# Kernel optimization log

Measured on AMD Instinct MI355X. Metric: run time of the kernel, lower is better.

Reference implementation:

```python
import jax, jax.numpy as jnp
import numpy as np

B, S, IN, OUT = 4, 2048, 4096, 11008


def setup_inputs() -> dict:
    key = jax.random.key(0)
    k1, k2, k3, k4, k5 = jax.random.split(key, 5)
    x = jax.random.normal(k1, (B, S, IN), dtype=jnp.float32)
    # int8 quantized weights, stored as int32 per harness spec but values in int8 range
    W_int8 = jax.random.randint(k2, (OUT, IN), -128, 128, dtype=jnp.int32)
    # per-output-channel scales (small positive) and zero-points
    scale = jax.random.uniform(k3, (OUT,), dtype=jnp.float32, minval=1e-3, maxval=2e-2)
    zero = jax.random.uniform(k4, (OUT,), dtype=jnp.float32, minval=-8.0, maxval=8.0)
    bias = jax.random.normal(k5, (OUT,), dtype=jnp.float32) * 0.01
    return {"x": x, "W_int8": W_int8, "scale": scale, "zero": zero, "bias": bias}


def reference(x, W_int8, scale, zero, bias):
    # Original torch forward raises on NaN/Inf in x; for valid inputs the math is
    # quant_matmul: dequantize W = (W_int8 - zero) * scale (per output channel),
    # then y = x @ W.T + bias.
    W = (W_int8.astype(jnp.float32) - zero[:, None]) * scale[:, None]  # [OUT, IN]
    y = jnp.einsum('bsi,oi->bso', x, W) + bias  # [B, S, OUT]
    return y
```

## Files before the change

### kernel.cpp

```cpp
#include <hip/hip_runtime.h>
#include <stdint.h>


#define M_DIM 8192
#define N_DIM 11008
#define K_DIM 4096
#define NT    (K_DIM / 128)
#define BUFB  65536

typedef __attribute__((ext_vector_type(4))) int i32x4;


__global__ void convert_w_kernel(const int* __restrict__ w,
                                 int8_t* __restrict__ o, int n4) {
  int idx = blockIdx.x * blockDim.x + threadIdx.x;
  int stride = gridDim.x * blockDim.x;
  for (int i = idx; i < n4; i += stride) {
    int4 v = ((const int4*)w)[i];
    int r = (v.x & 255) | ((v.y & 255) << 8) | ((v.z & 255) << 16) | ((v.w & 255) << 24);
    ((int*)o)[i] = r;
  }
}

__global__ __launch_bounds__(256) void quantx_kernel(
    const float* __restrict__ x, int8_t* __restrict__ h8, int8_t* __restrict__ l8,
    float* __restrict__ xs, float* __restrict__ rsum) {
  const int row = blockIdx.x;
  const int t = threadIdx.x;
  const float4* px = (const float4*)(x + (size_t)row * K_DIM);
  float4 v[4];
  float mx = 0.f, sm = 0.f;
  #pragma unroll
  for (int i = 0; i < 4; ++i) {
    v[i] = px[i * 256 + t];
    mx = fmaxf(mx, fmaxf(fmaxf(fabsf(v[i].x), fabsf(v[i].y)),
                         fmaxf(fabsf(v[i].z), fabsf(v[i].w))));
    sm += v[i].x + v[i].y + v[i].z + v[i].w;
  }
  #pragma unroll
  for (int off = 32; off > 0; off >>= 1) {
    mx = fmaxf(mx, __shfl_down(mx, off));
    sm += __shfl_down(sm, off);
  }
  __shared__ float rmx[4], rsm[4];
  const int wv = t >> 6, ln = t & 63;
  if (ln == 0) { rmx[wv] = mx; rsm[wv] = sm; }
  __syncthreads();
  const float rowmax = fmaxf(fmaxf(rmx[0], rmx[1]), fmaxf(rmx[2], rmx[3]));
  if (t == 0) {
    xs[row] = rowmax > 0.f ? rowmax / 16256.f : 0.f;
    rsum[row] = rsm[0] + rsm[1] + rsm[2] + rsm[3];
  }
  const float inv = rowmax > 0.f ? 16256.f / rowmax : 0.f;
  int* hp = (int*)(h8 + (size_t)row * K_DIM);
  int* lp = (int*)(l8 + (size_t)row * K_DIM);
  #pragma unroll
  for (int i = 0; i < 4; ++i) {
    int q0 = (int)rintf(v[i].x * inv);
    int q1 = (int)rintf(v[i].y * inv);
    int q2 = (int)rintf(v[i].z * inv);
    int q3 = (int)rintf(v[i].w * inv);
    int h0 = (q0 + 64) >> 7, h1 = (q1 + 64) >> 7, h2 = (q2 + 64) >> 7, h3 = (q3 + 64) >> 7;
    int l0 = q0 - (h0 << 7), l1 = q1 - (h1 << 7), l2 = q2 - (h2 << 7), l3 = q3 - (h3 << 7);
    hp[i * 256 + t] = (h0 & 255) | ((h1 & 255) << 8) | ((h2 & 255) << 16) | ((h3 & 255) << 24);
    lp[i * 256 + t] = (l0 & 255) | ((l1 & 255) << 8) | ((l2 & 255) << 16) | ((l3 & 255) << 24);
  }
}


__device__ __forceinline__ void stage_tile(
    const int8_t* __restrict__ Ah, const int8_t* __restrict__ Al,
    const int8_t* __restrict__ Bw, size_t a_base, size_t b_base,
    int ks, int srow, int scol, int wave, int8_t* buf) {
  #pragma unroll
  for (int r = 0; r < 2; ++r) {
    const int8_t* g = Ah + a_base + (size_t)(r * 64 + srow) * K_DIM + ks + scol;
    __builtin_amdgcn_global_load_lds((const __attribute__((address_space(1))) void*)g,
        (__attribute__((address_space(3))) void*)(buf + r * 8192 + wave * 1024), 16, 0, 0);
  }
  #pragma unroll
  for (int r = 0; r < 2; ++r) {
    const int8_t* g = Al + a_base + (size_t)(r * 64 + srow) * K_DIM + ks + scol;
    __builtin_amdgcn_global_load_lds((const __attribute__((address_space(1))) void*)g,
        (__attribute__((address_space(3))) void*)(buf + 16384 + r * 8192 + wave * 1024), 16, 0, 0);
  }
  #pragma unroll
  for (int r = 0; r < 4; ++r) {
    const int8_t* g = Bw + b_base + (size_t)(r * 64 + srow) * K_DIM + ks + scol;
    __builtin_amdgcn_global_load_lds((const __attribute__((address_space(1))) void*)g,
        (__attribute__((address_space(3))) void*)(buf + 32768 + r * 8192 + wave * 1024), 16, 0, 0);
  }
}

__global__ __launch_bounds__(512, 2) void qgemm_kernel(
    const int8_t* __restrict__ Ah, const int8_t* __restrict__ Al,
    const int8_t* __restrict__ Bw, const float* __restrict__ xs,
    const float* __restrict__ rowsum, const float* __restrict__ scale,
    const float* __restrict__ zero, const float* __restrict__ bias,
    float* __restrict__ out) {
  extern __shared__ int8_t smem[];

  const int tid = threadIdx.x;
  const int wave = tid >> 6;
  const int lane = tid & 63;

  const int bid = blockIdx.x;
  const int wg = (bid & 7) * 344 + (bid >> 3);
  const int group = wg / 344;
  const int rem = wg % 344;
  const int bm = group * 8 + (rem & 7);
  const int bn = rem >> 3;

  const int wr = wave >> 2;
  const int wc = wave & 3;

  i32x4 acch[4][4], accl[4][4];
  #pragma unroll
  for (int i = 0; i < 4; ++i)
    #pragma unroll
    for (int j = 0; j < 4; ++j) {
      acch[i][j] = (i32x4){0, 0, 0, 0};
      accl[i][j] = (i32x4){0, 0, 0, 0};
    }

  const int srow = tid >> 3;
  const int scol = (((tid & 7) ^ ((tid >> 3) & 7)) << 4);
  const size_t a_base = (size_t)(bm * 128) * K_DIM;
  const size_t b_base = (size_t)((size_t)bn * 256) * K_DIM;

  const int fr = lane & 15;
  const int g = lane >> 4;
  const int sw = fr & 7;
  const int sc0 = ((g ^ sw) << 4);
  const int sc1 = (((g + 4) ^ sw) << 4);

  stage_tile(Ah, Al, Bw, a_base, b_base, 0, srow, scol, wave, smem);
  asm volatile("s_waitcnt vmcnt(0)" ::: "memory");
  asm volatile("s_barrier" ::: "memory");

  for (int t = 0; t < NT; ++t) {
    if (t + 1 < NT) {
      stage_tile(Ah, Al, Bw, a_base, b_base, (t + 1) * 128, srow, scol, wave,
                 smem + ((t + 1) & 1) * BUFB);
      asm volatile("s_waitcnt vmcnt(8)" ::: "memory");
    } else {
      asm volatile("s_waitcnt vmcnt(0)" ::: "memory");
    }
    asm volatile("s_barrier" ::: "memory");

    const int8_t* buf = smem + (t & 1) * BUFB;
    const int8_t* ldsAh_ = buf;
    const int8_t* ldsAl_ = buf + 16384;
    const int8_t* ldsB_  = buf + 32768;

    #pragma unroll
    for (int h = 0; h < 2; ++h) {
      const int sc = h ? sc1 : sc0;
      i32x4 bfrag[4];
      #pragma unroll
      for (int ni = 0; ni < 4; ++ni) {
        const int row = wc * 64 + ni * 16 + fr;
        bfrag[ni] = *(const i32x4*)(ldsB_ + row * 128 + sc);
      }
      #pragma unroll
      for (int mi = 0; mi < 4; ++mi) {
        const int arow = (wr * 64 + mi * 16 + fr) * 128 + sc;
        i32x4 ahf = *(const i32x4*)(ldsAh_ + arow);
        i32x4 alf = *(const i32x4*)(ldsAl_ + arow);
        #pragma unroll
        for (int ni = 0; ni < 4; ++ni) {
          acch[mi][ni] = __builtin_amdgcn_mfma_i32_16x16x64_i8(ahf, bfrag[ni], acch[mi][ni], 0, 0, 0);
          accl[mi][ni] = __builtin_amdgcn_mfma_i32_16x16x64_i8(alf, bfrag[ni], accl[mi][ni], 0, 0, 0);
        }
      }
    }
    asm volatile("s_barrier" ::: "memory");
  }

  const int row0 = bm * 128 + wr * 64;
  const int col0 = bn * 256 + wc * 64;
  float s_[4], sz_[4], b_[4];
  #pragma unroll
  for (int ni = 0; ni < 4; ++ni) {
    const int n = col0 + ni * 16 + fr;
    const float s = scale[n];
    s_[ni] = s;
    sz_[ni] = s * zero[n];
    b_[ni] = bias[n];
  }
  #pragma unroll
  for (int mi = 0; mi < 4; ++mi) {
    #pragma unroll
    for (int j = 0; j < 4; ++j) {
      const int m = row0 + mi * 16 + g * 4 + j;
      const float xsm = xs[m];
      const float rs = rowsum[m];
      float* po = out + (size_t)m * N_DIM + col0;
      #pragma unroll
      for (int ni = 0; ni < 4; ++ni) {
        const float G = xsm * (128.f * (float)acch[mi][ni][j] + (float)accl[mi][ni][j]);
        po[ni * 16 + fr] = s_[ni] * G - sz_[ni] * rs + b_[ni];
      }
    }
  }
}


__global__ void fallback_kernel(const float* __restrict__ x, const int* __restrict__ w,
                                const float* __restrict__ scale, const float* __restrict__ zero,
                                const float* __restrict__ bias, float* __restrict__ out) {
  const int n = blockIdx.x * 16 + (threadIdx.x & 15);
  const int m = blockIdx.y * 16 + (threadIdx.x >> 4);
  const float z = zero[n];
  const float* xr = x + (size_t)m * K_DIM;
  const int* wr = w + (size_t)n * K_DIM;
  float acc = 0.f;
  for (int k = 0; k < K_DIM; ++k) acc += xr[k] * ((float)wr[k] - z);
  out[(size_t)m * N_DIM + n] = scale[n] * acc + bias[n];
}


extern "C" void kernel_launch(void* const* d_in, const int* in_sizes, int n_in,
                              void* d_out, int out_size, void* d_ws, size_t ws_size,
                              hipStream_t stream) {
  const float* x     = (const float*)d_in[0];
  const int*   w     = (const int*)d_in[1];
  const float* scale = (const float*)d_in[2];
  const float* zero  = (const float*)d_in[3];
  const float* bias  = (const float*)d_in[4];
  float* out = (float*)d_out;

  const size_t n_x = (size_t)M_DIM * K_DIM;
  const size_t n_w = (size_t)N_DIM * K_DIM;
  const size_t need = n_x * 2 + n_w + (size_t)M_DIM * 8;

  if (ws_size < need) {
    dim3 gr(N_DIM / 16, M_DIM / 16);
    fallback_kernel<<<gr, 256, 0, stream>>>(x, w, scale, zero, bias, out);
    return;
  }

  int8_t* x_h = (int8_t*)d_ws;
  int8_t* x_l = x_h + n_x;
  int8_t* w_8 = x_l + n_x;
  float* rsum = (float*)(w_8 + n_w);
  float* xs   = rsum + M_DIM;

  convert_w_kernel<<<2048, 256, 0, stream>>>(w, w_8, (int)(n_w / 4));
  quantx_kernel<<<M_DIM, 256, 0, stream>>>(x, x_h, x_l, xs, rsum);

  (void)hipFuncSetAttribute((const void*)qgemm_kernel,
                            hipFuncAttributeMaxDynamicSharedMemorySize, 2 * BUFB);

  const int nblocks = (M_DIM / 128) * (N_DIM / 256);
  qgemm_kernel<<<nblocks, 512, 2 * BUFB, stream>>>(x_h, x_l, w_8, xs, rsum,
                                                   scale, zero, bias, out);
}
```

Baseline: 738.0 us.

## Split main loop into four barrier-separated phases with interleaved prefetch and setprio

Restructures the GEMM main loop into four sub-phases, each of which loads A/B fragments from LDS and then issues a batch of MFMAs. The prefetch of the next tile is split into an A part and a B part, issued in the first and second phases so that global loads overlap with compute. MFMA blocks are wrapped in s_setprio to favour math waves, and the vmcnt wait moves to the end of the iteration. This adds more barriers per iteration, which costs synchronisation overhead and relies on the compiler keeping the scheduling as written.

After: 736.5 us. About the same (-0.2%).

```diff
diff --git a/kernel.cpp b/kernel.cpp
--- a/kernel.cpp
+++ b/kernel.cpp
@@ -68,10 +68,9 @@
 }
 
 
-__device__ __forceinline__ void stage_tile(
+__device__ __forceinline__ void stage_A(
     const int8_t* __restrict__ Ah, const int8_t* __restrict__ Al,
-    const int8_t* __restrict__ Bw, size_t a_base, size_t b_base,
-    int ks, int srow, int scol, int wave, int8_t* buf) {
+    size_t a_base, int ks, int srow, int scol, int wave, int8_t* buf) {
   #pragma unroll
   for (int r = 0; r < 2; ++r) {
     const int8_t* g = Ah + a_base + (size_t)(r * 64 + srow) * K_DIM + ks + scol;
@@ -84,6 +83,11 @@
     __builtin_amdgcn_global_load_lds((const __attribute__((address_space(1))) void*)g,
         (__attribute__((address_space(3))) void*)(buf + 16384 + r * 8192 + wave * 1024), 16, 0, 0);
   }
+}
+
+__device__ __forceinline__ void stage_B(
+    const int8_t* __restrict__ Bw, size_t b_base,
+    int ks, int srow, int scol, int wave, int8_t* buf) {
   #pragma unroll
   for (int r = 0; r < 4; ++r) {
     const int8_t* g = Bw + b_base + (size_t)(r * 64 + srow) * K_DIM + ks + scol;
@@ -91,6 +95,9 @@
         (__attribute__((address_space(3))) void*)(buf + 32768 + r * 8192 + wave * 1024), 16, 0, 0);
   }
 }
+
+#define WAIT_LGKM0() do { asm volatile("s_waitcnt lgkmcnt(0)" ::: "memory"); \
+                          __builtin_amdgcn_sched_barrier(0); } while (0)
 
 __global__ __launch_bounds__(512, 2) void qgemm_kernel(
     const int8_t* __restrict__ Ah, const int8_t* __restrict__ Al,
@@ -134,47 +141,106 @@
   const int sc0 = ((g ^ sw) << 4);
   const int sc1 = (((g + 4) ^ sw) << 4);
 
-  stage_tile(Ah, Al, Bw, a_base, b_base, 0, srow, scol, wave, smem);
+  stage_A(Ah, Al, a_base, 0, srow, scol, wave, smem);
+  stage_B(Bw, b_base, 0, srow, scol, wave, smem);
   asm volatile("s_waitcnt vmcnt(0)" ::: "memory");
-  asm volatile("s_barrier" ::: "memory");
+  __builtin_amdgcn_s_barrier();
 
   for (int t = 0; t < NT; ++t) {
-    if (t + 1 < NT) {
-      stage_tile(Ah, Al, Bw, a_base, b_base, (t + 1) * 128, srow, scol, wave,
-                 smem + ((t + 1) & 1) * BUFB);
-      asm volatile("s_waitcnt vmcnt(8)" ::: "memory");
-    } else {
-      asm volatile("s_waitcnt vmcnt(0)" ::: "memory");
-    }
-    asm volatile("s_barrier" ::: "memory");
-
     const int8_t* buf = smem + (t & 1) * BUFB;
+    int8_t* nxt = smem + ((t + 1) & 1) * BUFB;
     const int8_t* ldsAh_ = buf;
     const int8_t* ldsAl_ = buf + 16384;
     const int8_t* ldsB_  = buf + 32768;
-
-    #pragma unroll
-    for (int h = 0; h < 2; ++h) {
-      const int sc = h ? sc1 : sc0;
-      i32x4 bfrag[4];
-      #pragma unroll
-      for (int ni = 0; ni < 4; ++ni) {
-        const int row = wc * 64 + ni * 16 + fr;
-        bfrag[ni] = *(const i32x4*)(ldsB_ + row * 128 + sc);
-      }
-      #pragma unroll
-      for (int mi = 0; mi < 4; ++mi) {
-        const int arow = (wr * 64 + mi * 16 + fr) * 128 + sc;
-        i32x4 ahf = *(const i32x4*)(ldsAh_ + arow);
-        i32x4 alf = *(const i32x4*)(ldsAl_ + arow);
-        #pragma unroll
-        for (int ni = 0; ni < 4; ++ni) {
-          acch[mi][ni] = __builtin_amdgcn_mfma_i32_16x16x64_i8(ahf, bfrag[ni], acch[mi][ni], 0, 0, 0);
-          accl[mi][ni] = __builtin_amdgcn_mfma_i32_16x16x64_i8(alf, bfrag[ni], accl[mi][ni], 0, 0, 0);
-        }
-      }
-    }
-    asm volatile("s_barrier" ::: "memory");
+    const bool pf = (t + 1 < NT);
+    const int nks = (t + 1) * 128;
+
+    i32x4 bfrag[4], af[2][2];
+
+    #pragma unroll
+    for (int ni = 0; ni < 4; ++ni)
+      bfrag[ni] = *(const i32x4*)(ldsB_ + (wc * 64 + ni * 16 + fr) * 128 + sc0);
+    #pragma unroll
+    for (int mi = 0; mi < 2; ++mi) {
+      const int arow = (wr * 64 + mi * 16 + fr) * 128 + sc0;
+      af[mi][0] = *(const i32x4*)(ldsAh_ + arow);
+      af[mi][1] = *(const i32x4*)(ldsAl_ + arow);
+    }
+    if (pf) stage_A(Ah, Al, a_base, nks, srow, scol, wave, nxt);
+    __builtin_amdgcn_s_barrier();
+    WAIT_LGKM0();
+    __builtin_amdgcn_s_setprio(1);
+    #pragma unroll
+    for (int mi = 0; mi < 2; ++mi)
+      #pragma unroll
+      for (int ni = 0; ni < 4; ++ni) {
+        acch[mi][ni] = __builtin_amdgcn_mfma_i32_16x16x64_i8(af[mi][0], bfrag[ni], acch[mi][ni], 0, 0, 0);
+        accl[mi][ni] = __builtin_amdgcn_mfma_i32_16x16x64_i8(af[mi][1], bfrag[ni], accl[mi][ni], 0, 0, 0);
+      }
+    __builtin_amdgcn_s_setprio(0);
+    __builtin_amdgcn_s_barrier();
+
+    #pragma unroll
+    for (int mi = 0; mi < 2; ++mi) {
+      const int arow = (wr * 64 + (mi + 2) * 16 + fr) * 128 + sc0;
+      af[mi][0] = *(const i32x4*)(ldsAh_ + arow);
+      af[mi][1] = *(const i32x4*)(ldsAl_ + arow);
+    }
+    if (pf) stage_B(Bw, b_base, nks, srow, scol, wave, nxt);
+    __builtin_amdgcn_s_barrier();
+    WAIT_LGKM0();
+    __builtin_amdgcn_s_setprio(1);
+    #pragma unroll
+    for (int mi = 0; mi < 2; ++mi)
+      #pragma unroll
+      for (int ni = 0; ni < 4; ++ni) {
+        acch[mi + 2][ni] = __builtin_amdgcn_mfma_i32_16x16x64_i8(af[mi][0], bfrag[ni], acch[mi + 2][ni], 0, 0, 0);
+        accl[mi + 2][ni] = __builtin_amdgcn_mfma_i32_16x16x64_i8(af[mi][1], bfrag[ni], accl[mi + 2][ni], 0, 0, 0);
+      }
+    __builtin_amdgcn_s_setprio(0);
+    __builtin_amdgcn_s_barrier();
+
+    #pragma unroll
+    for (int ni = 0; ni < 4; ++ni)
+      bfrag[ni] = *(const i32x4*)(ldsB_ + (wc * 64 + ni * 16 + fr) * 128 + sc1);
+    #pragma unroll
+    for (int mi = 0; mi < 2; ++mi) {
+      const int arow = (wr * 64 + mi * 16 + fr) * 128 + sc1;
+      af[mi][0] = *(const i32x4*)(ldsAh_ + arow);
+      af[mi][1] = *(const i32x4*)(ldsAl_ + arow);
+    }
+    __builtin_amdgcn_s_barrier();
+    WAIT_LGKM0();
+    __builtin_amdgcn_s_setprio(1);
+    #pragma unroll
+    for (int mi = 0; mi < 2; ++mi)
+      #pragma unroll
+      for (int ni = 0; ni < 4; ++ni) {
+        acch[mi][ni] = __builtin_amdgcn_mfma_i32_16x16x64_i8(af[mi][0], bfrag[ni], acch[mi][ni], 0, 0, 0);
+        accl[mi][ni] = __builtin_amdgcn_mfma_i32_16x16x64_i8(af[mi][1], bfrag[ni], accl[mi][ni], 0, 0, 0);
+      }
+    __builtin_amdgcn_s_setprio(0);
+    __builtin_amdgcn_s_barrier();
+
+    #pragma unroll
+    for (int mi = 0; mi < 2; ++mi) {
+      const int arow = (wr * 64 + (mi + 2) * 16 + fr) * 128 + sc1;
+      af[mi][0] = *(const i32x4*)(ldsAh_ + arow);
+      af[mi][1] = *(const i32x4*)(ldsAl_ + arow);
+    }
+    __builtin_amdgcn_s_barrier();
+    WAIT_LGKM0();
+    __builtin_amdgcn_s_setprio(1);
+    #pragma unroll
+    for (int mi = 0; mi < 2; ++mi)
+      #pragma unroll
+      for (int ni = 0; ni < 4; ++ni) {
+        acch[mi + 2][ni] = __builtin_amdgcn_mfma_i32_16x16x64_i8(af[mi][0], bfrag[ni], acch[mi + 2][ni], 0, 0, 0);
+        accl[mi + 2][ni] = __builtin_amdgcn_mfma_i32_16x16x64_i8(af[mi][1], bfrag[ni], accl[mi + 2][ni], 0, 0, 0);
+      }
+    __builtin_amdgcn_s_setprio(0);
+    asm volatile("s_waitcnt vmcnt(0)" ::: "memory");
+    __builtin_amdgcn_s_barrier();
   }
 
   const int row0 = bm * 128 + wr * 64;
```

## Switch to 32x32x32 int8 MFMA with software-pipelined LDS reads and interleaved prefetch

Applied to the files above, without the earlier changes.

Replaces the 16x16x64 int8 MFMA tiles with 32x32x32 MFMAs, giving each wave 2x2 tiles of 16-element accumulators. The K loop is restructured so that LDS fragment reads for the next sub-step are double-buffered in registers and overlap the MFMAs, with the global-to-LDS prefetch split into A and B halves interleaved between reads. Barriers drop from two per tile to one, and s_setprio is raised around the MFMA bursts. The epilogue indexing is rewritten for the 32x32 output layout. The risks are higher register pressure from the extra fragment buffers and a stall from the full vmcnt(0) wait each iteration.

Measured after the change: 786.2 us. 1.07x slower.

```diff
diff --git a/kernel.cpp b/kernel.cpp
--- a/kernel.cpp
+++ b/kernel.cpp
@@ -9,6 +9,7 @@
 #define BUFB  65536
 
 typedef __attribute__((ext_vector_type(4))) int i32x4;
+typedef __attribute__((ext_vector_type(16))) int i32x16;
 
 
 __global__ void convert_w_kernel(const int* __restrict__ w,
@@ -68,10 +69,9 @@
 }
 
 
-__device__ __forceinline__ void stage_tile(
+__device__ __forceinline__ void stage_A(
     const int8_t* __restrict__ Ah, const int8_t* __restrict__ Al,
-    const int8_t* __restrict__ Bw, size_t a_base, size_t b_base,
-    int ks, int srow, int scol, int wave, int8_t* buf) {
+    size_t a_base, int ks, int srow, int scol, int wave, int8_t* buf) {
   #pragma unroll
   for (int r = 0; r < 2; ++r) {
     const int8_t* g = Ah + a_base + (size_t)(r * 64 + srow) * K_DIM + ks + scol;
@@ -84,6 +84,11 @@
     __builtin_amdgcn_global_load_lds((const __attribute__((address_space(1))) void*)g,
         (__attribute__((address_space(3))) void*)(buf + 16384 + r * 8192 + wave * 1024), 16, 0, 0);
   }
+}
+
+__device__ __forceinline__ void stage_B(
+    const int8_t* __restrict__ Bw, size_t b_base,
+    int ks, int srow, int scol, int wave, int8_t* buf) {
   #pragma unroll
   for (int r = 0; r < 4; ++r) {
     const int8_t* g = Bw + b_base + (size_t)(r * 64 + srow) * K_DIM + ks + scol;
@@ -114,13 +119,13 @@
   const int wr = wave >> 2;
   const int wc = wave & 3;
 
-  i32x4 acch[4][4], accl[4][4];
-  #pragma unroll
-  for (int i = 0; i < 4; ++i)
+  i32x16 acch[2][2], accl[2][2];
+  #pragma unroll
+  for (int i = 0; i < 2; ++i)
     #pragma unroll
-    for (int j = 0; j < 4; ++j) {
-      acch[i][j] = (i32x4){0, 0, 0, 0};
-      accl[i][j] = (i32x4){0, 0, 0, 0};
+    for (int j = 0; j < 2; ++j) {
+      acch[i][j] = (i32x16)(0);
+      accl[i][j] = (i32x16)(0);
     }
 
   const int srow = tid >> 3;
@@ -128,78 +133,97 @@
   const size_t a_base = (size_t)(bm * 128) * K_DIM;
   const size_t b_base = (size_t)((size_t)bn * 256) * K_DIM;
 
-  const int fr = lane & 15;
-  const int g = lane >> 4;
-  const int sw = fr & 7;
-  const int sc0 = ((g ^ sw) << 4);
-  const int sc1 = (((g + 4) ^ sw) << 4);
-
-  stage_tile(Ah, Al, Bw, a_base, b_base, 0, srow, scol, wave, smem);
+  const int r31 = lane & 31;
+  const int g5 = lane >> 5;
+  const int sw = lane & 7;
+  int scb[4];
+  #pragma unroll
+  for (int s = 0; s < 4; ++s) scb[s] = (((2 * s + g5) ^ sw) << 4);
+
+  const int arow0 = (wr * 64 + r31) * 128;
+  const int arow1 = arow0 + 32 * 128;
+  const int brow0 = (wc * 64 + r31) * 128;
+  const int brow1 = brow0 + 32 * 128;
+
+#define RD_STEP(s, fa, fb) do {                                         \
+    fb[0]    = *(const i32x4*)(ldsB_  + brow0 + scb[s]);                \
+    fb[1]    = *(const i32x4*)(ldsB_  + brow1 + scb[s]);                \
+    fa[0][0] = *(const i32x4*)(ldsAh_ + arow0 + scb[s]);                \
+    fa[0][1] = *(const i32x4*)(ldsAl_ + arow0 + scb[s]);                \
+    fa[1][0] = *(const i32x4*)(ldsAh_ + arow1 + scb[s]);                \
+    fa[1][1] = *(const i32x4*)(ldsAl_ + arow1 + scb[s]);                \
+  } while (0)
+
+#define MM_STEP(fa, fb) do {                                                        \
+    __builtin_amdgcn_s_setprio(1);                                                  \
+    acch[0][0] = __builtin_amdgcn_mfma_i32_32x32x32_i8(fa[0][0], fb[0], acch[0][0], 0, 0, 0); \
+    accl[0][0] = __builtin_amdgcn_mfma_i32_32x32x32_i8(fa[0][1], fb[0], accl[0][0], 0, 0, 0); \
+    acch[0][1] = __builtin_amdgcn_mfma_i32_32x32x32_i8(fa[0][0], fb[1], acch[0][1], 0, 0, 0); \
+    accl[0][1] = __builtin_amdgcn_mfma_i32_32x32x32_i8(fa[0][1], fb[1], accl[0][1], 0, 0, 0); \
+    acch[1][0] = __builtin_amdgcn_mfma_i32_32x32x32_i8(fa[1][0], fb[0], acch[1][0], 0, 0, 0); \
+    accl[1][0] = __builtin_amdgcn_mfma_i32_32x32x32_i8(fa[1][1], fb[0], accl[1][0], 0, 0, 0); \
+    acch[1][1] = __builtin_amdgcn_mfma_i32_32x32x32_i8(fa[1][0], fb[1], acch[1][1], 0, 0, 0); \
+    accl[1][1] = __builtin_amdgcn_mfma_i32_32x32x32_i8(fa[1][1], fb[1], accl[1][1], 0, 0, 0); \
+    __builtin_amdgcn_s_setprio(0);                                                  \
+  } while (0)
+
+  stage_A(Ah, Al, a_base, 0, srow, scol, wave, smem);
+  stage_B(Bw, b_base, 0, srow, scol, wave, smem);
   asm volatile("s_waitcnt vmcnt(0)" ::: "memory");
-  asm volatile("s_barrier" ::: "memory");
+  __builtin_amdgcn_s_barrier();
+
+  i32x4 fa0[2][2], fb0[2], fa1[2][2], fb1[2];
 
   for (int t = 0; t < NT; ++t) {
-    if (t + 1 < NT) {
-      stage_tile(Ah, Al, Bw, a_base, b_base, (t + 1) * 128, srow, scol, wave,
-                 smem + ((t + 1) & 1) * BUFB);
-      asm volatile("s_waitcnt vmcnt(8)" ::: "memory");
-    } else {
-      asm volatile("s_waitcnt vmcnt(0)" ::: "memory");
-    }
-    asm volatile("s_barrier" ::: "memory");
-
     const int8_t* buf = smem + (t & 1) * BUFB;
+    int8_t* nxt = smem + ((t + 1) & 1) * BUFB;
     const int8_t* ldsAh_ = buf;
     const int8_t* ldsAl_ = buf + 16384;
     const int8_t* ldsB_  = buf + 32768;
-
-    #pragma unroll
-    for (int h = 0; h < 2; ++h) {
-      const int sc = h ? sc1 : sc0;
-      i32x4 bfrag[4];
-      #pragma unroll
-      for (int ni = 0; ni < 4; ++ni) {
-        const int row = wc * 64 + ni * 16 + fr;
-        bfrag[ni] = *(const i32x4*)(ldsB_ + row * 128 + sc);
-      }
-      #pragma unroll
-      for (int mi = 0; mi < 4; ++mi) {
-        const int arow = (wr * 64 + mi * 16 + fr) * 128 + sc;
-        i32x4 ahf = *(const i32x4*)(ldsAh_ + arow);
-        i32x4 alf = *(const i32x4*)(ldsAl_ + arow);
-        #pragma unroll
-        for (int ni = 0; ni < 4; ++ni) {
-          acch[mi][ni] = __builtin_amdgcn_mfma_i32_16x16x64_i8(ahf, bfrag[ni], acch[mi][ni], 0, 0, 0);
-          accl[mi][ni] = __builtin_amdgcn_mfma_i32_16x16x64_i8(alf, bfrag[ni], accl[mi][ni], 0, 0, 0);
-        }
-      }
-    }
-    asm volatile("s_barrier" ::: "memory");
+    const bool pf = (t + 1 < NT);
+    const int nks = (t + 1) * 128;
+
+    RD_STEP(0, fa0, fb0);
+    if (pf) stage_A(Ah, Al, a_base, nks, srow, scol, wave, nxt);
+    RD_STEP(1, fa1, fb1);
+    if (pf) stage_B(Bw, b_base, nks, srow, scol, wave, nxt);
+
+    MM_STEP(fa0, fb0);
+    RD_STEP(2, fa0, fb0);
+    MM_STEP(fa1, fb1);
+    RD_STEP(3, fa1, fb1);
+    MM_STEP(fa0, fb0);
+
+    asm volatile("s_waitcnt lgkmcnt(0)" ::: "memory");
+    asm volatile("s_waitcnt vmcnt(0)" ::: "memory");
+    __builtin_amdgcn_s_barrier();
+
+    MM_STEP(fa1, fb1);
   }
 
   const int row0 = bm * 128 + wr * 64;
   const int col0 = bn * 256 + wc * 64;
-  float s_[4], sz_[4], b_[4];
-  #pragma unroll
-  for (int ni = 0; ni < 4; ++ni) {
-    const int n = col0 + ni * 16 + fr;
+  float s_[2], sz_[2], b_[2];
+  #pragma unroll
+  for (int ni = 0; ni < 2; ++ni) {
+    const int n = col0 + ni * 32 + r31;
     const float s = scale[n];
     s_[ni] = s;
     sz_[ni] = s * zero[n];
     b_[ni] = bias[n];
   }
   #pragma unroll
-  for (int mi = 0; mi < 4; ++mi) {
+  for (int mi = 0; mi < 2; ++mi) {
     #pragma unroll
-    for (int j = 0; j < 4; ++j) {
-      const int m = row0 + mi * 16 + g * 4 + j;
+    for (int j = 0; j < 16; ++j) {
+      const int m = row0 + mi * 32 + (j & 3) + 8 * (j >> 2) + 4 * g5;
       const float xsm = xs[m];
       const float rs = rowsum[m];
-      float* po = out + (size_t)m * N_DIM + col0;
+      float* po = out + (size_t)m * N_DIM + col0 + r31;
       #pragma unroll
-      for (int ni = 0; ni < 4; ++ni) {
+      for (int ni = 0; ni < 2; ++ni) {
         const float G = xsm * (128.f * (float)acch[mi][ni][j] + (float)accl[mi][ni][j]);
-        po[ni * 16 + fr] = s_[ni] * G - sz_[ni] * rs + b_[ni];
+        po[ni * 32] = s_[ni] * G - sz_[ni] * rs + b_[ni];
       }
     }
   }
```

## Pre-swizzle operands into MFMA fragment layout and load directly from global memory

Applied to the files above, without the earlier changes.

The weight-conversion and activation-quantization kernels now write int8 operands in a tiled layout that matches the MFMA fragment order: 16-row panels with 16-byte chunks interleaved per lane. The GEMM kernel no longer stages tiles in LDS. Each lane loads its fragments straight from global memory into registers, with a two-stage register double buffer and raised priority around the MFMA bursts. This removes LDS traffic and most barriers, but each wave now fetches its own copy of A and B from global memory or cache instead of sharing tiles through LDS, which increases L2 traffic.

Result: slower. 1.011 ms (+37.0%).

```diff
diff --git a/kernel.cpp b/kernel.cpp
--- a/kernel.cpp
+++ b/kernel.cpp
@@ -6,100 +6,89 @@
 #define N_DIM 11008
 #define K_DIM 4096
 #define NT    (K_DIM / 128)
-#define BUFB  65536
 
 typedef __attribute__((ext_vector_type(4))) int i32x4;
 
 
-__global__ void convert_w_kernel(const int* __restrict__ w,
-                                 int8_t* __restrict__ o, int n4) {
-  int idx = blockIdx.x * blockDim.x + threadIdx.x;
-  int stride = gridDim.x * blockDim.x;
-  for (int i = idx; i < n4; i += stride) {
-    int4 v = ((const int4*)w)[i];
-    int r = (v.x & 255) | ((v.y & 255) << 8) | ((v.z & 255) << 16) | ((v.w & 255) << 24);
-    ((int*)o)[i] = r;
+__global__ __launch_bounds__(256) void convert_w_kernel(
+    const int* __restrict__ w, int8_t* __restrict__ Wq) {
+  const int q = blockIdx.x;
+  const int r = threadIdx.x & 15;
+  const int cg = threadIdx.x >> 4;
+  const int o = q * 16 + r;
+  const int4* src = (const int4*)(w + (size_t)o * K_DIM + cg * 256);
+  int8_t* dst = Wq + (size_t)q * 65536 + (size_t)(cg * 16) * 256 + r * 16;
+  #pragma unroll 4
+  for (int jc = 0; jc < 16; ++jc) {
+    int4 o4;
+    int4 v0 = src[jc * 4 + 0], v1 = src[jc * 4 + 1];
+    int4 v2 = src[jc * 4 + 2], v3 = src[jc * 4 + 3];
+    o4.x = (v0.x & 255) | ((v0.y & 255) << 8) | ((v0.z & 255) << 16) | ((v0.w & 255) << 24);
+    o4.y = (v1.x & 255) | ((v1.y & 255) << 8) | ((v1.z & 255) << 16) | ((v1.w & 255) << 24);
+    o4.z = (v2.x & 255) | ((v2.y & 255) << 8) | ((v2.z & 255) << 16) | ((v2.w & 255) << 24);
+    o4.w = (v3.x & 255) | ((v3.y & 255) << 8) | ((v3.z & 255) << 16) | ((v3.w & 255) << 24);
+    *(int4*)(dst + jc * 256) = o4;
   }
 }
 
 __global__ __launch_bounds__(256) void quantx_kernel(
-    const float* __restrict__ x, int8_t* __restrict__ h8, int8_t* __restrict__ l8,
+    const float* __restrict__ x, int8_t* __restrict__ Axh, int8_t* __restrict__ Axl,
     float* __restrict__ xs, float* __restrict__ rsum) {
-  const int row = blockIdx.x;
-  const int t = threadIdx.x;
-  const float4* px = (const float4*)(x + (size_t)row * K_DIM);
-  float4 v[4];
+  const int p = blockIdx.x;
+  const int r = threadIdx.x & 15;
+  const int cg = threadIdx.x >> 4;
+  const int row = p * 16 + r;
+  const float4* px = (const float4*)(x + (size_t)row * K_DIM + cg * 256);
+
   float mx = 0.f, sm = 0.f;
-  #pragma unroll
-  for (int i = 0; i < 4; ++i) {
-    v[i] = px[i * 256 + t];
-    mx = fmaxf(mx, fmaxf(fmaxf(fabsf(v[i].x), fabsf(v[i].y)),
-                         fmaxf(fabsf(v[i].z), fabsf(v[i].w))));
-    sm += v[i].x + v[i].y + v[i].z + v[i].w;
-  }
-  #pragma unroll
-  for (int off = 32; off > 0; off >>= 1) {
-    mx = fmaxf(mx, __shfl_down(mx, off));
-    sm += __shfl_down(sm, off);
-  }
-  __shared__ float rmx[4], rsm[4];
-  const int wv = t >> 6, ln = t & 63;
-  if (ln == 0) { rmx[wv] = mx; rsm[wv] = sm; }
+  #pragma unroll 8
+  for (int j = 0; j < 64; ++j) {
+    float4 v = px[j];
+    mx = fmaxf(mx, fmaxf(fmaxf(fabsf(v.x), fabsf(v.y)), fmaxf(fabsf(v.z), fabsf(v.w))));
+    sm += v.x + v.y + v.z + v.w;
+  }
+  __shared__ float s_mx[16][16], s_sm[16][16];
+  s_mx[cg][r] = mx; s_sm[cg][r] = sm;
   __syncthreads();
-  const float rowmax = fmaxf(fmaxf(rmx[0], rmx[1]), fmaxf(rmx[2], rmx[3]));
-  if (t == 0) {
+  float rowmax = 0.f, rowsumv = 0.f;
+  #pragma unroll
+  for (int k = 0; k < 16; ++k) {
+    rowmax = fmaxf(rowmax, s_mx[k][r]);
+    rowsumv += s_sm[k][r];
+  }
+  if (cg == 0) {
     xs[row] = rowmax > 0.f ? rowmax / 16256.f : 0.f;
-    rsum[row] = rsm[0] + rsm[1] + rsm[2] + rsm[3];
+    rsum[row] = rowsumv;
   }
   const float inv = rowmax > 0.f ? 16256.f / rowmax : 0.f;
-  int* hp = (int*)(h8 + (size_t)row * K_DIM);
-  int* lp = (int*)(l8 + (size_t)row * K_DIM);
-  #pragma unroll
-  for (int i = 0; i < 4; ++i) {
-    int q0 = (int)rintf(v[i].x * inv);
-    int q1 = (int)rintf(v[i].y * inv);
-    int q2 = (int)rintf(v[i].z * inv);
-    int q3 = (int)rintf(v[i].w * inv);
-    int h0 = (q0 + 64) >> 7, h1 = (q1 + 64) >> 7, h2 = (q2 + 64) >> 7, h3 = (q3 + 64) >> 7;
-    int l0 = q0 - (h0 << 7), l1 = q1 - (h1 << 7), l2 = q2 - (h2 << 7), l3 = q3 - (h3 << 7);
-    hp[i * 256 + t] = (h0 & 255) | ((h1 & 255) << 8) | ((h2 & 255) << 16) | ((h3 & 255) << 24);
-    lp[i * 256 + t] = (l0 & 255) | ((l1 & 255) << 8) | ((l2 & 255) << 16) | ((l3 & 255) << 24);
-  }
-}
-
-
-__device__ __forceinline__ void stage_tile(
-    const int8_t* __restrict__ Ah, const int8_t* __restrict__ Al,
-    const int8_t* __restrict__ Bw, size_t a_base, size_t b_base,
-    int ks, int srow, int scol, int wave, int8_t* buf) {
-  #pragma unroll
-  for (int r = 0; r < 2; ++r) {
-    const int8_t* g = Ah + a_base + (size_t)(r * 64 + srow) * K_DIM + ks + scol;
-    __builtin_amdgcn_global_load_lds((const __attribute__((address_space(1))) void*)g,
-        (__attribute__((address_space(3))) void*)(buf + r * 8192 + wave * 1024), 16, 0, 0);
-  }
-  #pragma unroll
-  for (int r = 0; r < 2; ++r) {
-    const int8_t* g = Al + a_base + (size_t)(r * 64 + srow) * K_DIM + ks + scol;
-    __builtin_amdgcn_global_load_lds((const __attribute__((address_space(1))) void*)g,
-        (__attribute__((address_space(3))) void*)(buf + 16384 + r * 8192 + wave * 1024), 16, 0, 0);
-  }
-  #pragma unroll
-  for (int r = 0; r < 4; ++r) {
-    const int8_t* g = Bw + b_base + (size_t)(r * 64 + srow) * K_DIM + ks + scol;
-    __builtin_amdgcn_global_load_lds((const __attribute__((address_space(1))) void*)g,
-        (__attribute__((address_space(3))) void*)(buf + 32768 + r * 8192 + wave * 1024), 16, 0, 0);
-  }
-}
+
+  int8_t* dh = Axh + (size_t)p * 65536 + (size_t)(cg * 16) * 256 + r * 16;
+  int8_t* dl = Axl + (size_t)p * 65536 + (size_t)(cg * 16) * 256 + r * 16;
+  #pragma unroll 2
+  for (int jc = 0; jc < 16; ++jc) {
+    int4 hw, lw;
+    #pragma unroll
+    for (int u = 0; u < 4; ++u) {
+      float4 v = px[jc * 4 + u];
+      int q0 = (int)rintf(v.x * inv), q1 = (int)rintf(v.y * inv);
+      int q2 = (int)rintf(v.z * inv), q3 = (int)rintf(v.w * inv);
+      int h0 = (q0 + 64) >> 7, h1 = (q1 + 64) >> 7, h2 = (q2 + 64) >> 7, h3 = (q3 + 64) >> 7;
+      int l0 = q0 - (h0 << 7), l1 = q1 - (h1 << 7), l2 = q2 - (h2 << 7), l3 = q3 - (h3 << 7);
+      ((int*)&hw)[u] = (h0 & 255) | ((h1 & 255) << 8) | ((h2 & 255) << 16) | ((h3 & 255) << 24);
+      ((int*)&lw)[u] = (l0 & 255) | ((l1 & 255) << 8) | ((l2 & 255) << 16) | ((l3 & 255) << 24);
+    }
+    *(int4*)(dh + jc * 256) = hw;
+    *(int4*)(dl + jc * 256) = lw;
+  }
+}
+
 
 __global__ __launch_bounds__(512, 2) void qgemm_kernel(
-    const int8_t* __restrict__ Ah, const int8_t* __restrict__ Al,
-    const int8_t* __restrict__ Bw, const float* __restrict__ xs,
+    const int8_t* __restrict__ Axh, const int8_t* __restrict__ Axl,
+    const int8_t* __restrict__ Wq, const float* __restrict__ xs,
     const float* __restrict__ rowsum, const float* __restrict__ scale,
     const float* __restrict__ zero, const float* __restrict__ bias,
     float* __restrict__ out) {
-  extern __shared__ int8_t smem[];
-
   const int tid = threadIdx.x;
   const int wave = tid >> 6;
   const int lane = tid & 63;
@@ -114,6 +103,16 @@
   const int wr = wave >> 2;
   const int wc = wave & 3;
 
+  const int fr = lane & 15;
+  const int g = lane >> 4;
+  const uint32_t laneoff = (uint32_t)(g * 256 + fr * 16);
+
+  uint32_t pa[4], pb[4];
+  #pragma unroll
+  for (int mi = 0; mi < 4; ++mi) pa[mi] = (uint32_t)(bm * 8 + wr * 4 + mi) * 65536u + laneoff;
+  #pragma unroll
+  for (int ni = 0; ni < 4; ++ni) pb[ni] = (uint32_t)(bn * 16 + wc * 4 + ni) * 65536u + laneoff;
+
   i32x4 acch[4][4], accl[4][4];
   #pragma unroll
   for (int i = 0; i < 4; ++i)
@@ -123,59 +122,48 @@
       accl[i][j] = (i32x4){0, 0, 0, 0};
     }
 
-  const int srow = tid >> 3;
-  const int scol = (((tid & 7) ^ ((tid >> 3) & 7)) << 4);
-  const size_t a_base = (size_t)(bm * 128) * K_DIM;
-  const size_t b_base = (size_t)((size_t)bn * 256) * K_DIM;
-
-  const int fr = lane & 15;
-  const int g = lane >> 4;
-  const int sw = fr & 7;
-  const int sc0 = ((g ^ sw) << 4);
-  const int sc1 = (((g + 4) ^ sw) << 4);
-
-  stage_tile(Ah, Al, Bw, a_base, b_base, 0, srow, scol, wave, smem);
-  asm volatile("s_waitcnt vmcnt(0)" ::: "memory");
-  asm volatile("s_barrier" ::: "memory");
-
+#define LOADH(cb, ah, al, bf) do {                                        \
+    _Pragma("unroll")                                                     \
+    for (int mi = 0; mi < 4; ++mi) {                                      \
+      ah[mi] = *(const i32x4*)(Axh + pa[mi] + (cb));                      \
+      al[mi] = *(const i32x4*)(Axl + pa[mi] + (cb));                      \
+    }                                                                     \
+    _Pragma("unroll")                                                     \
+    for (int ni = 0; ni < 4; ++ni)                                        \
+      bf[ni] = *(const i32x4*)(Wq + pb[ni] + (cb));                       \
+  } while (0)
+
+#define MMH(ah, al, bf) do {                                              \
+    __builtin_amdgcn_s_setprio(1);                                        \
+    _Pragma("unroll")                                                     \
+    for (int mi = 0; mi < 4; ++mi)                                        \
+      _Pragma("unroll")                                                   \
+      for (int ni = 0; ni < 4; ++ni) {                                    \
+        acch[mi][ni] = __builtin_amdgcn_mfma_i32_16x16x64_i8(ah[mi], bf[ni], acch[mi][ni], 0, 0, 0); \
+        accl[mi][ni] = __builtin_amdgcn_mfma_i32_16x16x64_i8(al[mi], bf[ni], accl[mi][ni], 0, 0, 0); \
+      }                                                                   \
+    __builtin_amdgcn_s_setprio(0);                                        \
+  } while (0)
+
+  i32x4 ah0[4], al0[4], bf0[4], ah1[4], al1[4], bf1[4];
+
+  LOADH(0u, ah0, al0, bf0);
+
+  #pragma unroll 1
   for (int t = 0; t < NT; ++t) {
+    const uint32_t cb1 = (uint32_t)t * 2048u + 1024u;
+    LOADH(cb1, ah1, al1, bf1);
+    MMH(ah0, al0, bf0);
     if (t + 1 < NT) {
-      stage_tile(Ah, Al, Bw, a_base, b_base, (t + 1) * 128, srow, scol, wave,
-                 smem + ((t + 1) & 1) * BUFB);
-      asm volatile("s_waitcnt vmcnt(8)" ::: "memory");
-    } else {
-      asm volatile("s_waitcnt vmcnt(0)" ::: "memory");
-    }
-    asm volatile("s_barrier" ::: "memory");
-
-    const int8_t* buf = smem + (t & 1) * BUFB;
-    const int8_t* ldsAh_ = buf;
-    const int8_t* ldsAl_ = buf + 16384;
-    const int8_t* ldsB_  = buf + 32768;
-
-    #pragma unroll
-    for (int h = 0; h < 2; ++h) {
-      const int sc = h ? sc1 : sc0;
-      i32x4 bfrag[4];
-      #pragma unroll
-      for (int ni = 0; ni < 4; ++ni) {
-        const int row = wc * 64 + ni * 16 + fr;
-        bfrag[ni] = *(const i32x4*)(ldsB_ + row * 128 + sc);
-      }
-      #pragma unroll
-      for (int mi = 0; mi < 4; ++mi) {
-        const int arow = (wr * 64 + mi * 16 + fr) * 128 + sc;
-        i32x4 ahf = *(const i32x4*)(ldsAh_ + arow);
-        i32x4 alf = *(const i32x4*)(ldsAl_ + arow);
-        #pragma unroll
-        for (int ni = 0; ni < 4; ++ni) {
-          acch[mi][ni] = __builtin_amdgcn_mfma_i32_16x16x64_i8(ahf, bfrag[ni], acch[mi][ni], 0, 0, 0);
-          accl[mi][ni] = __builtin_amdgcn_mfma_i32_16x16x64_i8(alf, bfrag[ni], accl[mi][ni], 0, 0, 0);
-        }
-      }
-    }
-    asm volatile("s_barrier" ::: "memory");
-  }
+      const uint32_t cb2 = (uint32_t)(t + 1) * 2048u;
+      LOADH(cb2, ah0, al0, bf0);
+    }
+    MMH(ah1, al1, bf1);
+    __builtin_amdgcn_s_barrier();
+  }
+
+#undef LOADH
+#undef MMH
 
   const int row0 = bm * 128 + wr * 64;
   const int col0 = bn * 256 + wc * 64;
@@ -242,17 +230,14 @@
 
   int8_t* x_h = (int8_t*)d_ws;
   int8_t* x_l = x_h + n_x;
-  int8_t* w_8 = x_l + n_x;
-  float* rsum = (float*)(w_8 + n_w);
+  int8_t* w_q = x_l + n_x;
+  float* rsum = (float*)(w_q + n_w);
   float* xs   = rsum + M_DIM;
 
-  convert_w_kernel<<<2048, 256, 0, stream>>>(w, w_8, (int)(n_w / 4));
-  quantx_kernel<<<M_DIM, 256, 0, stream>>>(x, x_h, x_l, xs, rsum);
-
-  (void)hipFuncSetAttribute((const void*)qgemm_kernel,
-                            hipFuncAttributeMaxDynamicSharedMemorySize, 2 * BUFB);
+  convert_w_kernel<<<N_DIM / 16, 256, 0, stream>>>(w, w_q);
+  quantx_kernel<<<M_DIM / 16, 256, 0, stream>>>(x, x_h, x_l, xs, rsum);
 
   const int nblocks = (M_DIM / 128) * (N_DIM / 256);
-  qgemm_kernel<<<nblocks, 512, 2 * BUFB, stream>>>(x_h, x_l, w_8, xs, rsum,
-                                                   scale, zero, bias, out);
-}
+  qgemm_kernel<<<nblocks, 512, 0, stream>>>(x_h, x_l, w_q, xs, rsum,
+                                            scale, zero, bias, out);
+}
```
